# Performance work log

Measured on AMD Instinct MI355X. Metric: run time of the kernel, lower is better.

Reference implementation:

```python
import jax, jax.numpy as jnp
import numpy as np

T, N, K, E = 5, 2048, 20, 512
H, AI, BL, G1, G2, U = 64, 32, 64, 64, 64, 8
SLOPE, ALPHA = 0.01, 1.0


def gru(x, Wih, Whh, bih, bhh):
    # batch_first torch nn.GRU with h0 = 0. x: [B, L, I] -> [B, L, Hd]
    Hd = Whh.shape[1]
    def step(h, xt):
        gi = xt @ Wih.T + bih
        gh = h @ Whh.T + bhh
        ir, iz, in_ = jnp.split(gi, 3, axis=-1)
        hr, hz, hn = jnp.split(gh, 3, axis=-1)
        r = jax.nn.sigmoid(ir + hr)
        z = jax.nn.sigmoid(iz + hz)
        n = jnp.tanh(in_ + r * hn)
        h_new = (1.0 - z) * n + z * h
        return h_new, h_new
    h0 = jnp.zeros((x.shape[0], Hd), x.dtype)
    _, ys = jax.lax.scan(step, h0, jnp.swapaxes(x, 0, 1))
    return jnp.swapaxes(ys, 0, 1)


def lin_attn(x, w1, b1, w2):
    # LinearAttention: softmax over dim=2 (weights_size=1), then bmm -> [B,1,H]
    inter = jnp.tanh(x @ w1.T + b1)
    w = jax.nn.softmax(inter @ w2.T, axis=2)  # [B,L,1]
    return jnp.einsum('blk,blh->bkh', w, x)


def sgat_multi(x, W, a, adj):
    # All U SGAT heads at once. Decompose a^T [Wh_i || Wh_j] = s1_i + s2_j
    # (same math as the dense NxNx2F construction, without materializing it).
    O = W.shape[-1]
    Wh = jnp.einsum('nf,ufo->uno', x, W)                 # [U,N,O]
    s1 = jnp.einsum('uno,uo->un', Wh, a[:, :O, 0])
    s2 = jnp.einsum('uno,uo->un', Wh, a[:, O:, 0])
    e = jax.nn.leaky_relu(s1[:, :, None] + s2[:, None, :], SLOPE)  # [U,N,N]
    e = jnp.where(adj[None, :, :] > 0, e, -9e15)
    att = jax.nn.softmax(e, axis=2)
    h = jnp.einsum('unm,umo->uno', att, Wh)              # [U,N,O]
    # torch.cat over heads along feature dim -> [N, U*O]
    return jnp.transpose(h, (1, 0, 2)).reshape(x.shape[0], -1)


def setup_inputs() -> dict:
    key = jax.random.key(0)
    ks = iter(jax.random.split(key, 40))
    def nrm(shape, scale=0.1):
        return jax.random.normal(next(ks), shape, dtype=jnp.float32) * scale
    d = {}
    d['p'] = nrm((N, T, 3), 1.0)
    d['m'] = nrm((T, N, K, E), 1.0)
    adj = (jax.random.uniform(next(ks), (N, N)) < 0.05).astype(jnp.float32)
    d['adj'] = jnp.maximum(adj, jnp.eye(N, dtype=jnp.float32))
    d['Wih_p'] = nrm((3 * H, 3)); d['Whh_p'] = nrm((3 * H, H))
    d['bih_p'] = nrm((3 * H,)); d['bhh_p'] = nrm((3 * H,))
    d['Wih_m'] = nrm((3 * H, E)); d['Whh_m'] = nrm((3 * H, H))
    d['bih_m'] = nrm((3 * H,)); d['bhh_m'] = nrm((3 * H,))
    d['Wih_s'] = nrm((3 * H, H)); d['Whh_s'] = nrm((3 * H, H))
    d['bih_s'] = nrm((3 * H,)); d['bhh_s'] = nrm((3 * H,))
    for pref in ('ap', 'am', 'as'):
        d[pref + '_w1'] = nrm((AI, H)); d[pref + '_b1'] = nrm((AI,))
        d[pref + '_w2'] = nrm((1, AI))
    d['blend_W'] = nrm((BL, H, H)); d['blend_b'] = nrm((BL,))
    d['g1_W'] = nrm((U, BL, G1)); d['g1_a'] = nrm((U, 2 * G1, 1))
    d['g2_W'] = nrm((U, U * G1, G2)); d['g2_a'] = nrm((U, 2 * G2, 1))
    d['fin_W'] = nrm((1, U * G2)); d['fin_b'] = nrm((1,))
    return d


def reference(p, m, adj, Wih_p, Whh_p, bih_p, bhh_p, Wih_m, Whh_m, bih_m, bhh_m,
              Wih_s, Whh_s, bih_s, bhh_s, ap_w1, ap_b1, ap_w2, am_w1, am_b1, am_w2,
              as_w1, as_b1, as_w2, blend_W, blend_b, g1_W, g1_a, g2_W, g2_a,
              fin_W, fin_b):
    h_p = gru(p, Wih_p, Whh_p, bih_p, bhh_p)                     # [N,T,H]
    q = lin_attn(h_p, ap_w1, ap_b1, ap_w2)                       # [N,1,H]
    # all T message-days through gru_m at once (equivalent to python loop)
    h_m = gru(m.reshape(T * N, K, E), Wih_m, Whh_m, bih_m, bhh_m)
    r = lin_attn(h_m, am_w1, am_b1, am_w2).reshape(T, N, H).transpose(1, 0, 2)
    h_s = gru(r, Wih_s, Whh_s, bih_s, bhh_s)                     # [N,T,H]
    c = lin_attn(h_s, as_w1, as_b1, as_w2)                       # [N,1,H]
    # Blend: bilinear + relu
    x = jax.nn.relu(jnp.einsum('nbi,oij,nbj->nbo', q, blend_W, c) + blend_b)
    x = x.reshape(N, BL)
    z = jax.nn.elu(sgat_multi(x, g1_W, g1_a, adj), ALPHA)        # [N,U*G1]
    new_z = jax.nn.sigmoid(sgat_multi(z, g2_W, g2_a, adj))       # [N,U*G2]
    return jax.nn.sigmoid(new_z @ fin_W.T + fin_b)               # [N,1]
```

## Files before the change

### kernel.cpp

```cpp
#include <hip/hip_runtime.h>
#include <math.h>

namespace {

constexpr int T = 5, N = 2048, K = 20, E = 512;
constexpr int H = 64, U = 8;
constexpr int CAP = 512;
constexpr float SLOPE = 0.01f;

typedef __attribute__((ext_vector_type(8))) short short8;
typedef __attribute__((ext_vector_type(4))) float f32x4;

__device__ inline float sigm(float x) { return 1.0f / (1.0f + expf(-x)); }

__device__ inline void bsplit(float x, short& hi, short& lo) {
  unsigned u = __float_as_uint(x);
  hi = (short)(u >> 16);
  float r = x - __uint_as_float(u & 0xFFFF0000u);
  lo = (short)(__float_as_uint(r) >> 16);
}

__device__ inline float rdlane(float v, int lane) {
  return __int_as_float(__builtin_amdgcn_readlane(__float_as_int(v), lane));
}

__device__ inline void pack512(const float* __restrict__ src, short* __restrict__ dst,
                               const int Ksz, const int pb, const int nPB) {
  const int nb64 = Ksz >> 6;
  const int total = 8 * Ksz * 64;
  for (int idx = threadIdx.x + pb * 256; idx < total; idx += 256 * nPB) {
    const int u = idx / (Ksz * 64), rem = idx - u * Ksz * 64;
    const int f = rem >> 6, o = rem & 63;
    const int col = u * 64 + o;
    const long base = ((long)(col >> 7) * nb64 + (f >> 6)) * 8192
                    + (((f >> 5) & 1) * 8 + ((col >> 4) & 7)) * 512
                    + ((f >> 3) & 3) * 128 + (col & 15) * 8 + (f & 7);
    dst[base] = (short)(__float_as_uint(src[idx]) >> 16);
  }
}

__global__ __launch_bounds__(256) void k_prep_all(
    const float* __restrict__ WihM, const float* __restrict__ WhhM,
    const float* __restrict__ WihS, const float* __restrict__ WhhS,
    const float* __restrict__ WhhP, const float* __restrict__ Wb,
    const float* __restrict__ g1W, const float* __restrict__ g2W,
    const float* __restrict__ adj,
    short* __restrict__ BfM, short* __restrict__ BfS,
    short* __restrict__ Bf1, short* __restrict__ Bf2,
    float* __restrict__ WhhTm, float* __restrict__ WhhTs, float* __restrict__ WhhTp,
    float* __restrict__ Wt2, int* __restrict__ nbr, int* __restrict__ deg)
{
  const int b = blockIdx.x;
  if (b < N / 4) {
    const int w = threadIdx.x >> 6, lane = threadIdx.x & 63;
    const int i = b * 4 + w;
    int base = 0;
    for (int j0 = 0; j0 < N; j0 += 64) {
      const float v = adj[(long)i * N + j0 + lane];
      const unsigned long long mask = __ballot(v > 0.f);
      const int pre = __popcll(mask & ((1ull << lane) - 1ull));
      if (v > 0.f && base + pre < CAP) nbr[i * CAP + base + pre] = j0 + lane;
      base += __popcll(mask);
    }
    if (lane == 0) deg[i] = base < CAP ? base : CAP;
    return;
  }
  const int pb = b - N / 4;
  constexpr int NPB = 128;
  for (int idx = threadIdx.x + pb * 256; idx < 192 * 512; idx += 256 * NPB) {
    const int o = idx >> 9, k = idx & 511;
    const long base = (long)(k >> 6) * 12288 + (((k >> 5) & 1) * 12 + (o >> 4)) * 512
                    + ((k >> 3) & 3) * 128 + (o & 15) * 8 + (k & 7);
    BfM[base] = (short)(__float_as_uint(WihM[idx]) >> 16);
  }
  for (int idx = threadIdx.x + pb * 256; idx < 192 * 64; idx += 256 * NPB) {
    const int o = idx >> 6, k = idx & 63;
    const long base = (((k >> 5) & 1) * 12 + (o >> 4)) * 512
                    + ((k >> 3) & 3) * 128 + (o & 15) * 8 + (k & 7);
    BfS[base] = (short)(__float_as_uint(WihS[idx]) >> 16);
  }
  for (int idx = threadIdx.x + pb * 256; idx < 64 * 192; idx += 256 * NPB) {
    const int k2 = idx / 192, row = idx % 192;
    WhhTm[idx] = WhhM[row * 64 + k2];
    WhhTs[idx] = WhhS[row * 64 + k2];
    WhhTp[idx] = WhhP[row * 64 + k2];
  }
  for (int idx = threadIdx.x + pb * 256; idx < 64 * 64 * 64; idx += 256 * NPB) {
    const int o = idx >> 12, rem = idx & 4095, i = rem >> 6, j = rem & 63;
    Wt2[((i * 16 + (j >> 2)) * 64 + o) * 4 + (j & 3)] = Wb[(o * 64 + i) * 64 + j];
  }
  pack512(g1W, Bf1, 64, pb, NPB);
  pack512(g2W, Bf2, 512, pb, NPB);
}

__global__ __launch_bounds__(256, 3) void k_gemm(
    const float* __restrict__ A, const short* __restrict__ Bf,
    const float* __restrict__ bias, float* __restrict__ out,
    const long row0, const int nb, const int strideA)
{
  __shared__ alignas(16) short Bc[2][24 * 512];
  const int tid = threadIdx.x, w = tid >> 6, l = tid & 63;
  const int lr = l & 15, g = l >> 4;
  const long blkrow = (long)blockIdx.x * 128;

  f32x4 acc[2][12];
  #pragma unroll
  for (int mf = 0; mf < 2; ++mf)
    #pragma unroll
    for (int nt = 0; nt < 12; ++nt) acc[mf][nt] = (f32x4){0.f, 0.f, 0.f, 0.f};

  auto STAGE = [&](int buf, int b) {
    const short* __restrict__ bsrc = Bf + (long)b * 12288;
    #pragma unroll
    for (int i = 0; i < 6; ++i) {
      const int c = w + i * 4;
      __builtin_amdgcn_global_load_lds(
          (const __attribute__((address_space(1))) void*)(bsrc + c * 512 + l * 8),
          (__attribute__((address_space(3))) void*)(&Bc[buf][c * 512]), 16, 0, 0);
    }
  };

  STAGE(0, 0);
  __syncthreads();

  for (int b = 0; b < nb; ++b) {
    if (b + 1 < nb) STAGE((b + 1) & 1, b + 1);
    short8 ah[2][2], al[2][2];
    #pragma unroll
    for (int kc = 0; kc < 2; ++kc)
      #pragma unroll
      for (int mf = 0; mf < 2; ++mf) {
        const long r = blkrow + w * 32 + mf * 16 + lr;
        const float* __restrict__ src = A + (row0 + r) * (long)strideA + b * 64 + kc * 32 + g * 8;
        const float4 v0 = *reinterpret_cast<const float4*>(src);
        const float4 v1 = *reinterpret_cast<const float4*>(src + 4);
        short h0,l0,h1,l1,h2,l2,h3,l3,h4,l4,h5,l5,h6,l6,h7,l7;
        bsplit(v0.x,h0,l0); bsplit(v0.y,h1,l1); bsplit(v0.z,h2,l2); bsplit(v0.w,h3,l3);
        bsplit(v1.x,h4,l4); bsplit(v1.y,h5,l5); bsplit(v1.z,h6,l6); bsplit(v1.w,h7,l7);
        ah[kc][mf] = (short8){h0,h1,h2,h3,h4,h5,h6,h7};
        al[kc][mf] = (short8){l0,l1,l2,l3,l4,l5,l6,l7};
      }
    const short* __restrict__ bcur = &Bc[b & 1][0];
    #pragma unroll
    for (int kc = 0; kc < 2; ++kc) {
      #pragma unroll
      for (int nt = 0; nt < 12; ++nt) {
        const short8 bh = *reinterpret_cast<const short8*>(bcur + (kc * 12 + nt) * 512 + l * 8);
        #pragma unroll
        for (int mf = 0; mf < 2; ++mf) {
          acc[mf][nt] = __builtin_amdgcn_mfma_f32_16x16x32_bf16(ah[kc][mf], bh, acc[mf][nt], 0, 0, 0);
          acc[mf][nt] = __builtin_amdgcn_mfma_f32_16x16x32_bf16(al[kc][mf], bh, acc[mf][nt], 0, 0, 0);
        }
      }
    }
    __syncthreads();
  }

  #pragma unroll
  for (int mf = 0; mf < 2; ++mf) {
    const long rbase = blkrow + w * 32 + mf * 16 + g * 4;
    #pragma unroll
    for (int nt = 0; nt < 12; ++nt) {
      const int col = nt * 16 + lr;
      const float bb = bias[col];
      #pragma unroll
      for (int i = 0; i < 4; ++i)
        out[(rbase + i) * 192 + col] = acc[mf][nt][i] + bb;
    }
  }
}

__global__ __launch_bounds__(256, 3) void k_gemmW(
    const float* __restrict__ A, const short* __restrict__ Bf2,
    const float* __restrict__ ga,
    float* __restrict__ Wh, float* __restrict__ s1, float* __restrict__ s2,
    const int nb, const int strideA)
{
  __shared__ alignas(16) short Bc[2][16 * 512];
  const int tid = threadIdx.x, w = tid >> 6, l = tid & 63;
  const int lr = l & 15, g = l >> 4;
  const long blkrow = (long)blockIdx.x * 64;
  const int cb = blockIdx.y;

  f32x4 acc[8];
  #pragma unroll
  for (int nt = 0; nt < 8; ++nt) acc[nt] = (f32x4){0.f, 0.f, 0.f, 0.f};

  auto STAGE = [&](int buf, int b) {
    const short* __restrict__ bsrc = Bf2 + ((long)cb * nb + b) * 8192;
    #pragma unroll
    for (int i = 0; i < 4; ++i) {
      const int c = w + i * 4;
      __builtin_amdgcn_global_load_lds(
          (const __attribute__((address_space(1))) void*)(bsrc + c * 512 + l * 8),
          (__attribute__((address_space(3))) void*)(&Bc[buf][c * 512]), 16, 0, 0);
    }
  };

  STAGE(0, 0);
  __syncthreads();

  for (int b = 0; b < nb; ++b) {
    if (b + 1 < nb) STAGE((b + 1) & 1, b + 1);
    short8 ah[2], al[2];
    #pragma unroll
    for (int kc = 0; kc < 2; ++kc) {
      const long r = blkrow + w * 16 + lr;
      const float* __restrict__ src = A + r * (long)strideA + b * 64 + kc * 32 + g * 8;
      const float4 v0 = *reinterpret_cast<const float4*>(src);
      const float4 v1 = *reinterpret_cast<const float4*>(src + 4);
      short h0,l0,h1,l1,h2,l2,h3,l3,h4,l4,h5,l5,h6,l6,h7,l7;
      bsplit(v0.x,h0,l0); bsplit(v0.y,h1,l1); bsplit(v0.z,h2,l2); bsplit(v0.w,h3,l3);
      bsplit(v1.x,h4,l4); bsplit(v1.y,h5,l5); bsplit(v1.z,h6,l6); bsplit(v1.w,h7,l7);
      ah[kc] = (short8){h0,h1,h2,h3,h4,h5,h6,h7};
      al[kc] = (short8){l0,l1,l2,l3,l4,l5,l6,l7};
    }
    const short* __restrict__ bcur = &Bc[b & 1][0];
    #pragma unroll
    for (int kc = 0; kc < 2; ++kc) {
      #pragma unroll
      for (int nt = 0; nt < 8; ++nt) {
        const short8 bh = *reinterpret_cast<const short8*>(bcur + (kc * 8 + nt) * 512 + l * 8);
        acc[nt] = __builtin_amdgcn_mfma_f32_16x16x32_bf16(ah[kc], bh, acc[nt], 0, 0, 0);
        acc[nt] = __builtin_amdgcn_mfma_f32_16x16x32_bf16(al[kc], bh, acc[nt], 0, 0, 0);
      }
    }
    __syncthreads();
  }

  const long rbase = blkrow + w * 16 + g * 4;
  #pragma unroll
  for (int nt = 0; nt < 8; ++nt) {
    const int col = cb * 128 + nt * 16 + lr;
    const int u = col >> 6, o = col & 63;
    #pragma unroll
    for (int i = 0; i < 4; ++i)
      Wh[((long)u * N + (rbase + i)) * 64 + o] = acc[nt][i];
  }
  #pragma unroll
  for (int i = 0; i < 4; ++i) {
    const long r = rbase + i;
    #pragma unroll
    for (int uh = 0; uh < 2; ++uh) {
      const int u = cb * 2 + uh;
      float p1 = 0.f, p2 = 0.f;
      #pragma unroll
      for (int nt4 = 0; nt4 < 4; ++nt4) {
        const float v = acc[uh * 4 + nt4][i];
        const int o = nt4 * 16 + lr;
        p1 += v * ga[u * 128 + o];
        p2 += v * ga[u * 128 + 64 + o];
      }
      #pragma unroll
      for (int dd = 8; dd > 0; dd >>= 1) { p1 += __shfl_xor(p1, dd, 64); p2 += __shfl_xor(p2, dd, 64); }
      if (lr == 0) { s1[u * N + r] = p1; s2[u * N + r] = p2; }
    }
  }
}

__global__ __launch_bounds__(256, 2) void k_recur(
    const float* __restrict__ gi, const float* __restrict__ WhhT,
    const float* __restrict__ bhh, float* __restrict__ rout, const int seq0)
{
  const int tid = threadIdx.x, w = tid >> 6, l = tid & 63;
  const int lseq = blockIdx.x * 4 + w;
  float wr[64], wz[64], wn[64];
  #pragma unroll
  for (int k2 = 0; k2 < 64; ++k2) {
    wr[k2] = WhhT[k2 * 192 + l];
    wz[k2] = WhhT[k2 * 192 + 64 + l];
    wn[k2] = WhhT[k2 * 192 + 128 + l];
  }
  const float bR = bhh[l], bZ = bhh[64 + l], bN = bhh[128 + l];
  const float* __restrict__ grow = gi + (long)lseq * K * 192;
  float h = 0.f, rsum = 0.f;
  float gR = grow[l], gZ = grow[64 + l], gN = grow[128 + l];
  for (int k = 0; k < K; ++k) {
    float nR = 0.f, nZ = 0.f, nN = 0.f;
    if (k + 1 < K) {
      const int off = (k + 1) * 192;
      nR = grow[off + l]; nZ = grow[off + 64 + l]; nN = grow[off + 128 + l];
    }
    float aR = bR, aZ = bZ, aN = bN;
    #pragma unroll
    for (int k2 = 0; k2 < 64; ++k2) {
      const float hk = rdlane(h, k2);
      aR += wr[k2] * hk; aZ += wz[k2] * hk; aN += wn[k2] * hk;
    }
    const float r = sigm(gR + aR);
    const float z = sigm(gZ + aZ);
    const float nn = tanhf(gN + r * aN);
    h = (1.f - z) * nn + z * h;
    rsum += h;
    gR = nR; gZ = nZ; gN = nN;
  }
  const int gseq = seq0 + lseq;
  const int tt = gseq / N, n = gseq % N;
  rout[(n * T + tt) * H + l] = rsum;
}

__global__ __launch_bounds__(256, 2) void k_recur_p(
    const float* __restrict__ p, const float* __restrict__ Wih,
    const float* __restrict__ WhhT, const float* __restrict__ bih,
    const float* __restrict__ bhh, float* __restrict__ q)
{
  const int tid = threadIdx.x, w = tid >> 6, l = tid & 63;
  const int n = blockIdx.x * 4 + w;
  float wr[64], wz[64], wn[64];
  #pragma unroll
  for (int k2 = 0; k2 < 64; ++k2) {
    wr[k2] = WhhT[k2 * 192 + l];
    wz[k2] = WhhT[k2 * 192 + 64 + l];
    wn[k2] = WhhT[k2 * 192 + 128 + l];
  }
  float iR[3], iZ[3], iN[3];
  #pragma unroll
  for (int c = 0; c < 3; ++c) {
    iR[c] = Wih[l * 3 + c];
    iZ[c] = Wih[(64 + l) * 3 + c];
    iN[c] = Wih[(128 + l) * 3 + c];
  }
  const float biR = bih[l], biZ = bih[64 + l], biN = bih[128 + l];
  const float bhR = bhh[l], bhZ = bhh[64 + l], bhN = bhh[128 + l];
  float h = 0.f, qs = 0.f;
  for (int t = 0; t < T; ++t) {
    const float x0 = p[n * 15 + t * 3], x1 = p[n * 15 + t * 3 + 1], x2 = p[n * 15 + t * 3 + 2];
    const float gR = biR + iR[0] * x0 + iR[1] * x1 + iR[2] * x2;
    const float gZ = biZ + iZ[0] * x0 + iZ[1] * x1 + iZ[2] * x2;
    const float gN = biN + iN[0] * x0 + iN[1] * x1 + iN[2] * x2;
    float aR = bhR, aZ = bhZ, aN = bhN;
    #pragma unroll
    for (int k2 = 0; k2 < 64; ++k2) {
      const float hk = rdlane(h, k2);
      aR += wr[k2] * hk; aZ += wz[k2] * hk; aN += wn[k2] * hk;
    }
    const float r = sigm(gR + aR), z = sigm(gZ + aZ);
    const float nn = tanhf(gN + r * aN);
    h = (1.f - z) * nn + z * h;
    qs += h;
  }
  q[n * H + l] = qs;
}

__global__ __launch_bounds__(256, 2) void k_recur_s(
    const float* __restrict__ gx, const float* __restrict__ WhhT,
    const float* __restrict__ bhh, float* __restrict__ c)
{
  const int tid = threadIdx.x, w = tid >> 6, l = tid & 63;
  const int n = blockIdx.x * 4 + w;
  float wr[64], wz[64], wn[64];
  #pragma unroll
  for (int k2 = 0; k2 < 64; ++k2) {
    wr[k2] = WhhT[k2 * 192 + l];
    wz[k2] = WhhT[k2 * 192 + 64 + l];
    wn[k2] = WhhT[k2 * 192 + 128 + l];
  }
  const float bR = bhh[l], bZ = bhh[64 + l], bN = bhh[128 + l];
  const float* __restrict__ grow = gx + (long)n * T * 192;
  float h = 0.f, cs = 0.f;
  for (int t = 0; t < T; ++t) {
    const float gR = grow[t * 192 + l], gZ = grow[t * 192 + 64 + l], gN = grow[t * 192 + 128 + l];
    float aR = bR, aZ = bZ, aN = bN;
    #pragma unroll
    for (int k2 = 0; k2 < 64; ++k2) {
      const float hk = rdlane(h, k2);
      aR += wr[k2] * hk; aZ += wz[k2] * hk; aN += wn[k2] * hk;
    }
    const float r = sigm(gR + aR), z = sigm(gZ + aZ);
    const float nn = tanhf(gN + r * aN);
    h = (1.f - z) * nn + z * h;
    cs += h;
  }
  c[n * H + l] = cs;
}

__global__ __launch_bounds__(256) void k_blend(
    const float* __restrict__ q, const float* __restrict__ c,
    const float* __restrict__ Wt2, const float* __restrict__ b,
    float* __restrict__ xout)
{
  __shared__ float qs[8][64];
  __shared__ alignas(16) float cs[8][64];
  const int tid = threadIdx.x;
  const int o = tid & 63, grp = tid >> 6;
  const int n0 = blockIdx.x * 8;
  for (int idx = tid; idx < 512; idx += 256) {
    qs[idx >> 6][idx & 63] = q[(n0 + (idx >> 6)) * 64 + (idx & 63)];
    cs[idx >> 6][idx & 63] = c[(n0 + (idx >> 6)) * 64 + (idx & 63)];
  }
  __syncthreads();
  const int na = grp * 2, nb = na + 1;
  float acca = b[o], accb = b[o];
  const float4* __restrict__ W4 = reinterpret_cast<const float4*>(Wt2);
  const float4* ca4 = reinterpret_cast<const float4*>(&cs[na][0]);
  const float4* cb4 = reinterpret_cast<const float4*>(&cs[nb][0]);
  for (int i = 0; i < 64; ++i) {
    float pa = 0.f, pb = 0.f;
    #pragma unroll
    for (int j4 = 0; j4 < 16; ++j4) {
      const float4 wv = W4[(i * 16 + j4) * 64 + o];
      const float4 va = ca4[j4], vb = cb4[j4];
      pa += wv.x * va.x + wv.y * va.y + wv.z * va.z + wv.w * va.w;
      pb += wv.x * vb.x + wv.y * vb.y + wv.z * vb.z + wv.w * vb.w;
    }
    acca += qs[na][i] * pa;
    accb += qs[nb][i] * pb;
  }
  xout[(n0 + na) * 64 + o] = fmaxf(acca, 0.f);
  xout[(n0 + nb) * 64 + o] = fmaxf(accb, 0.f);
}

__global__ __launch_bounds__(256) void k_gat_attn(
    const float* __restrict__ Wh, const float* __restrict__ s1,
    const float* __restrict__ s2, const int* __restrict__ nbr,
    const int* __restrict__ deg, const int mode, float* __restrict__ out)
{
  __shared__ float ew[4][CAP];
  __shared__ int nb[4][CAP];
  const int w = threadIdx.x >> 6, lane = threadIdx.x & 63;
  const int row = blockIdx.x * 4 + w;
  const int u = row >> 11;
  const int i = row & (N - 1);
  const int d = deg[i];
  const float su = s1[u * N + i];
  float mx = -1e30f;
  for (int t = lane; t < d; t += 64) {
    const int j = nbr[i * CAP + t];
    float e = su + s2[u * N + j];
    e = e > 0.f ? e : SLOPE * e;
    ew[w][t] = e; nb[w][t] = j;
    mx = fmaxf(mx, e);
  }
  #pragma unroll
  for (int dd = 32; dd > 0; dd >>= 1) mx = fmaxf(mx, __shfl_xor(mx, dd, 64));
  float sm = 0.f;
  for (int t = lane; t < d; t += 64) {
    const float ex = expf(ew[w][t] - mx);
    ew[w][t] = ex;
    sm += ex;
  }
  #pragma unroll
  for (int dd = 32; dd > 0; dd >>= 1) sm += __shfl_xor(sm, dd, 64);
  __syncthreads();
  const float inv = 1.f / sm;
  float a0 = 0.f, a1 = 0.f, a2 = 0.f, a3 = 0.f;
  const float* __restrict__ whb = Wh + (long)u * N * 64 + lane;
  int t = 0;
  for (; t + 4 <= d; t += 4) {
    const float e0 = ew[w][t],     e1 = ew[w][t + 1];
    const float e2 = ew[w][t + 2], e3 = ew[w][t + 3];
    const int j0 = nb[w][t],     j1 = nb[w][t + 1];
    const int j2 = nb[w][t + 2], j3 = nb[w][t + 3];
    a0 += e0 * whb[(long)j0 * 64];
    a1 += e1 * whb[(long)j1 * 64];
    a2 += e2 * whb[(long)j2 * 64];
    a3 += e3 * whb[(long)j3 * 64];
  }
  for (; t < d; ++t) a0 += ew[w][t] * whb[(long)nb[w][t] * 64];
  float acc = ((a0 + a1) + (a2 + a3)) * inv;
  float val;
  if (mode == 0) val = acc > 0.f ? acc : (expf(acc) - 1.f);
  else           val = 1.f / (1.f + expf(-acc));
  out[(long)i * (U * 64) + u * 64 + lane] = val;
}

__global__ __launch_bounds__(256) void k_final(
    const float* __restrict__ nz, const float* __restrict__ fw,
    const float* __restrict__ fb, float* __restrict__ out)
{
  const int w = threadIdx.x >> 6, lane = threadIdx.x & 63;
  const int n = blockIdx.x * 4 + w;
  float p = 0.f;
  #pragma unroll
  for (int f = lane; f < 512; f += 64) p += nz[(long)n * 512 + f] * fw[f];
  #pragma unroll
  for (int d = 32; d > 0; d >>= 1) p += __shfl_xor(p, d, 64);
  if (lane == 0) out[n] = 1.f / (1.f + expf(-(p + fb[0])));
}

}

extern "C" void kernel_launch(void* const* d_in, const int* in_sizes, int n_in,
                              void* d_out, int out_size, void* d_ws, size_t ws_size,
                              hipStream_t stream)
{
  const float* p     = (const float*)d_in[0];
  const float* m     = (const float*)d_in[1];
  const float* adj   = (const float*)d_in[2];
  const float* Wih_p = (const float*)d_in[3];
  const float* Whh_p = (const float*)d_in[4];
  const float* bih_p = (const float*)d_in[5];
  const float* bhh_p = (const float*)d_in[6];
  const float* Wih_m = (const float*)d_in[7];
  const float* Whh_m = (const float*)d_in[8];
  const float* bih_m = (const float*)d_in[9];
  const float* bhh_m = (const float*)d_in[10];
  const float* Wih_s = (const float*)d_in[11];
  const float* Whh_s = (const float*)d_in[12];
  const float* bih_s = (const float*)d_in[13];
  const float* bhh_s = (const float*)d_in[14];
  const float* blend_W = (const float*)d_in[24];
  const float* blend_b = (const float*)d_in[25];
  const float* g1W = (const float*)d_in[26];
  const float* g1a = (const float*)d_in[27];
  const float* g2W = (const float*)d_in[28];
  const float* g2a = (const float*)d_in[29];
  const float* finW = (const float*)d_in[30];
  const float* finb = (const float*)d_in[31];

  float* ws = (float*)d_ws;
  float* q    = ws;
  float* rr   = q + N * H;
  float* c    = rr + N * T * H;
  float* xb   = c + N * H;
  float* Wh1  = xb + N * H;
  float* s1a  = Wh1 + U * N * 64;
  float* s2a  = s1a + U * N;
  float* z    = s2a + U * N;
  float* Wh2  = z + (long)N * 512;
  float* s1b  = Wh2 + U * N * 64;
  float* s2b  = s1b + U * N;
  float* nz   = s2b + U * N;
  float* Wt2  = nz + (long)N * 512;
  float* gx   = Wt2 + 64 * 64 * 64;
  float* WhhTm = gx + (long)10240 * 192;
  float* WhhTs = WhhTm + 64 * 192;
  float* WhhTp = WhhTs + 64 * 192;
  int*   nbr  = (int*)(WhhTp + 64 * 192);
  int*   deg  = nbr + (long)N * CAP;
  short* BfM  = (short*)(deg + N);
  short* BfS  = BfM + 8 * 12288;
  short* Bf1  = BfS + 12288;
  short* Bf2  = Bf1 + 4 * 8192;
  float* gi   = (float*)(Bf2 + 4 * 8 * 8192);

  const long avail = (long)(ws_size / 4) - (gi - ws);
  const long total_seqs = (long)T * N;
  long chunk = (avail / ((long)K * 192) / 32) * 32;
  if (chunk > total_seqs) chunk = total_seqs;
  if (chunk < 32) chunk = 32;

  k_prep_all<<<N / 4 + 128, 256, 0, stream>>>(
      Wih_m, Whh_m, Wih_s, Whh_s, Whh_p, blend_W, g1W, g2W, adj,
      BfM, BfS, Bf1, Bf2, WhhTm, WhhTs, WhhTp, Wt2, nbr, deg);
  k_recur_p<<<N / 4, 256, 0, stream>>>(p, Wih_p, WhhTp, bih_p, bhh_p, q);
  for (long s0 = 0; s0 < total_seqs; s0 += chunk) {
    const long cs = (total_seqs - s0) < chunk ? (total_seqs - s0) : chunk;
    const long rows = cs * K;
    k_gemm<<<(int)(rows / 128), 256, 0, stream>>>(m, BfM, bih_m, gi, s0 * K, 8, 512);
    k_recur<<<(int)(cs / 4), 256, 0, stream>>>(gi, WhhTm, bhh_m, rr, (int)s0);
  }
  k_gemm<<<80, 256, 0, stream>>>(rr, BfS, bih_s, gx, 0, 1, 64);
  k_recur_s<<<N / 4, 256, 0, stream>>>(gx, WhhTs, bhh_s, c);
  k_blend<<<N / 8, 256, 0, stream>>>(q, c, Wt2, blend_b, xb);
  k_gemmW<<<dim3(N / 64, 4), 256, 0, stream>>>(xb, Bf1, g1a, Wh1, s1a, s2a, 1, 64);
  k_gat_attn<<<(U * N) / 4, 256, 0, stream>>>(Wh1, s1a, s2a, nbr, deg, 0, z);
  k_gemmW<<<dim3(N / 64, 4), 256, 0, stream>>>(z, Bf2, g2a, Wh2, s1b, s2b, 8, 512);
  k_gat_attn<<<(U * N) / 4, 256, 0, stream>>>(Wh2, s1b, s2b, nbr, deg, 1, nz);
  k_final<<<N / 4, 256, 0, stream>>>(nz, finW, finb, (float*)d_out);
}
```

Measured before the change: 465.3 us.

## Fold p-GRU recurrence into prep kernel and prefetch A tiles in GEMMs

Removes the separate k_recur_p launch and runs the p-stream GRU as extra blocks of k_prep_all, reading Whh_p directly in row-major order instead of a transposed copy. The A-operand loads in k_gemm and k_gemmW are now software-prefetched into registers one k-block ahead, so global load latency can overlap the MFMA work. k_gemm launch bounds drop from 3 to 2 waves per EU to make room for the extra prefetch registers. The trade-off is lower occupancy, and the prep kernel becomes heavier and mixes register-hungry recurrence blocks with packing blocks.

```diff
diff --git a/kernel.cpp b/kernel.cpp
--- a/kernel.cpp
+++ b/kernel.cpp
@@ -45,10 +45,13 @@
     const float* __restrict__ WhhP, const float* __restrict__ Wb,
     const float* __restrict__ g1W, const float* __restrict__ g2W,
     const float* __restrict__ adj,
+    const float* __restrict__ p, const float* __restrict__ WihP,
+    const float* __restrict__ bihP, const float* __restrict__ bhhP,
     short* __restrict__ BfM, short* __restrict__ BfS,
     short* __restrict__ Bf1, short* __restrict__ Bf2,
-    float* __restrict__ WhhTm, float* __restrict__ WhhTs, float* __restrict__ WhhTp,
-    float* __restrict__ Wt2, int* __restrict__ nbr, int* __restrict__ deg)
+    float* __restrict__ WhhTm, float* __restrict__ WhhTs,
+    float* __restrict__ Wt2, int* __restrict__ nbr, int* __restrict__ deg,
+    float* __restrict__ q)
 {
   const int b = blockIdx.x;
   if (b < N / 4) {
@@ -65,35 +68,74 @@
     if (lane == 0) deg[i] = base < CAP ? base : CAP;
     return;
   }
-  const int pb = b - N / 4;
-  constexpr int NPB = 128;
-  for (int idx = threadIdx.x + pb * 256; idx < 192 * 512; idx += 256 * NPB) {
-    const int o = idx >> 9, k = idx & 511;
-    const long base = (long)(k >> 6) * 12288 + (((k >> 5) & 1) * 12 + (o >> 4)) * 512
-                    + ((k >> 3) & 3) * 128 + (o & 15) * 8 + (k & 7);
-    BfM[base] = (short)(__float_as_uint(WihM[idx]) >> 16);
-  }
-  for (int idx = threadIdx.x + pb * 256; idx < 192 * 64; idx += 256 * NPB) {
-    const int o = idx >> 6, k = idx & 63;
-    const long base = (((k >> 5) & 1) * 12 + (o >> 4)) * 512
-                    + ((k >> 3) & 3) * 128 + (o & 15) * 8 + (k & 7);
-    BfS[base] = (short)(__float_as_uint(WihS[idx]) >> 16);
-  }
-  for (int idx = threadIdx.x + pb * 256; idx < 64 * 192; idx += 256 * NPB) {
-    const int k2 = idx / 192, row = idx % 192;
-    WhhTm[idx] = WhhM[row * 64 + k2];
-    WhhTs[idx] = WhhS[row * 64 + k2];
-    WhhTp[idx] = WhhP[row * 64 + k2];
-  }
-  for (int idx = threadIdx.x + pb * 256; idx < 64 * 64 * 64; idx += 256 * NPB) {
-    const int o = idx >> 12, rem = idx & 4095, i = rem >> 6, j = rem & 63;
-    Wt2[((i * 16 + (j >> 2)) * 64 + o) * 4 + (j & 3)] = Wb[(o * 64 + i) * 64 + j];
-  }
-  pack512(g1W, Bf1, 64, pb, NPB);
-  pack512(g2W, Bf2, 512, pb, NPB);
-}
-
-__global__ __launch_bounds__(256, 3) void k_gemm(
+  if (b < N / 4 + 128) {
+    const int pb = b - N / 4;
+    constexpr int NPB = 128;
+    for (int idx = threadIdx.x + pb * 256; idx < 192 * 512; idx += 256 * NPB) {
+      const int o = idx >> 9, k = idx & 511;
+      const long base = (long)(k >> 6) * 12288 + (((k >> 5) & 1) * 12 + (o >> 4)) * 512
+                      + ((k >> 3) & 3) * 128 + (o & 15) * 8 + (k & 7);
+      BfM[base] = (short)(__float_as_uint(WihM[idx]) >> 16);
+    }
+    for (int idx = threadIdx.x + pb * 256; idx < 192 * 64; idx += 256 * NPB) {
+      const int o = idx >> 6, k = idx & 63;
+      const long base = (((k >> 5) & 1) * 12 + (o >> 4)) * 512
+                      + ((k >> 3) & 3) * 128 + (o & 15) * 8 + (k & 7);
+      BfS[base] = (short)(__float_as_uint(WihS[idx]) >> 16);
+    }
+    for (int idx = threadIdx.x + pb * 256; idx < 64 * 192; idx += 256 * NPB) {
+      const int k2 = idx / 192, row = idx % 192;
+      WhhTm[idx] = WhhM[row * 64 + k2];
+      WhhTs[idx] = WhhS[row * 64 + k2];
+    }
+    for (int idx = threadIdx.x + pb * 256; idx < 64 * 64 * 64; idx += 256 * NPB) {
+      const int o = idx >> 12, rem = idx & 4095, i = rem >> 6, j = rem & 63;
+      Wt2[((i * 16 + (j >> 2)) * 64 + o) * 4 + (j & 3)] = Wb[(o * 64 + i) * 64 + j];
+    }
+    pack512(g1W, Bf1, 64, pb, NPB);
+    pack512(g2W, Bf2, 512, pb, NPB);
+    return;
+  }
+  const int rb = b - (N / 4 + 128);
+  const int w = threadIdx.x >> 6, l = threadIdx.x & 63;
+  const int n = rb * 4 + w;
+  float wr[64], wz[64], wn[64];
+  #pragma unroll
+  for (int k2 = 0; k2 < 64; ++k2) {
+    wr[k2] = WhhP[l * 64 + k2];
+    wz[k2] = WhhP[(64 + l) * 64 + k2];
+    wn[k2] = WhhP[(128 + l) * 64 + k2];
+  }
+  float iR[3], iZ[3], iN[3];
+  #pragma unroll
+  for (int c = 0; c < 3; ++c) {
+    iR[c] = WihP[l * 3 + c];
+    iZ[c] = WihP[(64 + l) * 3 + c];
+    iN[c] = WihP[(128 + l) * 3 + c];
+  }
+  const float biR = bihP[l], biZ = bihP[64 + l], biN = bihP[128 + l];
+  const float bhR = bhhP[l], bhZ = bhhP[64 + l], bhN = bhhP[128 + l];
+  float h = 0.f, qs = 0.f;
+  for (int t = 0; t < T; ++t) {
+    const float x0 = p[n * 15 + t * 3], x1 = p[n * 15 + t * 3 + 1], x2 = p[n * 15 + t * 3 + 2];
+    const float gR = biR + iR[0] * x0 + iR[1] * x1 + iR[2] * x2;
+    const float gZ = biZ + iZ[0] * x0 + iZ[1] * x1 + iZ[2] * x2;
+    const float gN = biN + iN[0] * x0 + iN[1] * x1 + iN[2] * x2;
+    float aR = bhR, aZ = bhZ, aN = bhN;
+    #pragma unroll
+    for (int k2 = 0; k2 < 64; ++k2) {
+      const float hk = rdlane(h, k2);
+      aR += wr[k2] * hk; aZ += wz[k2] * hk; aN += wn[k2] * hk;
+    }
+    const float r = sigm(gR + aR), z = sigm(gZ + aZ);
+    const float nn = tanhf(gN + r * aN);
+    h = (1.f - z) * nn + z * h;
+    qs += h;
+  }
+  q[n * H + l] = qs;
+}
+
+__global__ __launch_bounds__(256, 2) void k_gemm(
     const float* __restrict__ A, const short* __restrict__ Bf,
     const float* __restrict__ bias, float* __restrict__ out,
     const long row0, const int nb, const int strideA)
@@ -109,6 +151,19 @@
     #pragma unroll
     for (int nt = 0; nt < 12; ++nt) acc[mf][nt] = (f32x4){0.f, 0.f, 0.f, 0.f};
 
+  float4 pf[2][2][2];
+
+  auto LOADA = [&](int b) {
+    #pragma unroll
+    for (int kc = 0; kc < 2; ++kc)
+      #pragma unroll
+      for (int mf = 0; mf < 2; ++mf) {
+        const long r = blkrow + w * 32 + mf * 16 + lr;
+        const float* __restrict__ src = A + (row0 + r) * (long)strideA + b * 64 + kc * 32 + g * 8;
+        pf[kc][mf][0] = *reinterpret_cast<const float4*>(src);
+        pf[kc][mf][1] = *reinterpret_cast<const float4*>(src + 4);
+      }
+  };
   auto STAGE = [&](int buf, int b) {
     const short* __restrict__ bsrc = Bf + (long)b * 12288;
     #pragma unroll
@@ -121,25 +176,25 @@
   };
 
   STAGE(0, 0);
+  LOADA(0);
   __syncthreads();
 
   for (int b = 0; b < nb; ++b) {
-    if (b + 1 < nb) STAGE((b + 1) & 1, b + 1);
+    const bool more = (b + 1 < nb);
+    if (more) STAGE((b + 1) & 1, b + 1);
     short8 ah[2][2], al[2][2];
     #pragma unroll
     for (int kc = 0; kc < 2; ++kc)
       #pragma unroll
       for (int mf = 0; mf < 2; ++mf) {
-        const long r = blkrow + w * 32 + mf * 16 + lr;
-        const float* __restrict__ src = A + (row0 + r) * (long)strideA + b * 64 + kc * 32 + g * 8;
-        const float4 v0 = *reinterpret_cast<const float4*>(src);
-        const float4 v1 = *reinterpret_cast<const float4*>(src + 4);
+        const float4 v0 = pf[kc][mf][0], v1 = pf[kc][mf][1];
         short h0,l0,h1,l1,h2,l2,h3,l3,h4,l4,h5,l5,h6,l6,h7,l7;
         bsplit(v0.x,h0,l0); bsplit(v0.y,h1,l1); bsplit(v0.z,h2,l2); bsplit(v0.w,h3,l3);
         bsplit(v1.x,h4,l4); bsplit(v1.y,h5,l5); bsplit(v1.z,h6,l6); bsplit(v1.w,h7,l7);
         ah[kc][mf] = (short8){h0,h1,h2,h3,h4,h5,h6,h7};
         al[kc][mf] = (short8){l0,l1,l2,l3,l4,l5,l6,l7};
       }
+    if (more) LOADA(b + 1);
     const short* __restrict__ bcur = &Bc[b & 1][0];
     #pragma unroll
     for (int kc = 0; kc < 2; ++kc) {
@@ -186,6 +241,17 @@
   #pragma unroll
   for (int nt = 0; nt < 8; ++nt) acc[nt] = (f32x4){0.f, 0.f, 0.f, 0.f};
 
+  float4 pf[2][2];
+
+  auto LOADA = [&](int b) {
+    #pragma unroll
+    for (int kc = 0; kc < 2; ++kc) {
+      const long r = blkrow + w * 16 + lr;
+      const float* __restrict__ src = A + r * (long)strideA + b * 64 + kc * 32 + g * 8;
+      pf[kc][0] = *reinterpret_cast<const float4*>(src);
+      pf[kc][1] = *reinterpret_cast<const float4*>(src + 4);
+    }
+  };
   auto STAGE = [&](int buf, int b) {
     const short* __restrict__ bsrc = Bf2 + ((long)cb * nb + b) * 8192;
     #pragma unroll
@@ -198,23 +264,23 @@
   };
 
   STAGE(0, 0);
+  LOADA(0);
   __syncthreads();
 
   for (int b = 0; b < nb; ++b) {
-    if (b + 1 < nb) STAGE((b + 1) & 1, b + 1);
+    const bool more = (b + 1 < nb);
+    if (more) STAGE((b + 1) & 1, b + 1);
     short8 ah[2], al[2];
     #pragma unroll
     for (int kc = 0; kc < 2; ++kc) {
-      const long r = blkrow + w * 16 + lr;
-      const float* __restrict__ src = A + r * (long)strideA + b * 64 + kc * 32 + g * 8;
-      const float4 v0 = *reinterpret_cast<const float4*>(src);
-      const float4 v1 = *reinterpret_cast<const float4*>(src + 4);
+      const float4 v0 = pf[kc][0], v1 = pf[kc][1];
       short h0,l0,h1,l1,h2,l2,h3,l3,h4,l4,h5,l5,h6,l6,h7,l7;
       bsplit(v0.x,h0,l0); bsplit(v0.y,h1,l1); bsplit(v0.z,h2,l2); bsplit(v0.w,h3,l3);
       bsplit(v1.x,h4,l4); bsplit(v1.y,h5,l5); bsplit(v1.z,h6,l6); bsplit(v1.w,h7,l7);
       ah[kc] = (short8){h0,h1,h2,h3,h4,h5,h6,h7};
       al[kc] = (short8){l0,l1,l2,l3,l4,l5,l6,l7};
     }
+    if (more) LOADA(b + 1);
     const short* __restrict__ bcur = &Bc[b & 1][0];
     #pragma unroll
     for (int kc = 0; kc < 2; ++kc) {
@@ -297,49 +363,6 @@
   const int gseq = seq0 + lseq;
   const int tt = gseq / N, n = gseq % N;
   rout[(n * T + tt) * H + l] = rsum;
-}
-
-__global__ __launch_bounds__(256, 2) void k_recur_p(
-    const float* __restrict__ p, const float* __restrict__ Wih,
-    const float* __restrict__ WhhT, const float* __restrict__ bih,
-    const float* __restrict__ bhh, float* __restrict__ q)
-{
-  const int tid = threadIdx.x, w = tid >> 6, l = tid & 63;
-  const int n = blockIdx.x * 4 + w;
-  float wr[64], wz[64], wn[64];
-  #pragma unroll
-  for (int k2 = 0; k2 < 64; ++k2) {
-    wr[k2] = WhhT[k2 * 192 + l];
-    wz[k2] = WhhT[k2 * 192 + 64 + l];
-    wn[k2] = WhhT[k2 * 192 + 128 + l];
-  }
-  float iR[3], iZ[3], iN[3];
-  #pragma unroll
-  for (int c = 0; c < 3; ++c) {
-    iR[c] = Wih[l * 3 + c];
-    iZ[c] = Wih[(64 + l) * 3 + c];
-    iN[c] = Wih[(128 + l) * 3 + c];
-  }
-  const float biR = bih[l], biZ = bih[64 + l], biN = bih[128 + l];
-  const float bhR = bhh[l], bhZ = bhh[64 + l], bhN = bhh[128 + l];
-  float h = 0.f, qs = 0.f;
-  for (int t = 0; t < T; ++t) {
-    const float x0 = p[n * 15 + t * 3], x1 = p[n * 15 + t * 3 + 1], x2 = p[n * 15 + t * 3 + 2];
-    const float gR = biR + iR[0] * x0 + iR[1] * x1 + iR[2] * x2;
-    const float gZ = biZ + iZ[0] * x0 + iZ[1] * x1 + iZ[2] * x2;
-    const float gN = biN + iN[0] * x0 + iN[1] * x1 + iN[2] * x2;
-    float aR = bhR, aZ = bhZ, aN = bhN;
-    #pragma unroll
-    for (int k2 = 0; k2 < 64; ++k2) {
-      const float hk = rdlane(h, k2);
-      aR += wr[k2] * hk; aZ += wz[k2] * hk; aN += wn[k2] * hk;
-    }
-    const float r = sigm(gR + aR), z = sigm(gZ + aZ);
-    const float nn = tanhf(gN + r * aN);
-    h = (1.f - z) * nn + z * h;
-    qs += h;
-  }
-  q[n * H + l] = qs;
 }
 
 __global__ __launch_bounds__(256, 2) void k_recur_s(
@@ -525,8 +548,7 @@
   float* gx   = Wt2 + 64 * 64 * 64;
   float* WhhTm = gx + (long)10240 * 192;
   float* WhhTs = WhhTm + 64 * 192;
-  float* WhhTp = WhhTs + 64 * 192;
-  int*   nbr  = (int*)(WhhTp + 64 * 192);
+  int*   nbr  = (int*)(WhhTs + 64 * 192);
   int*   deg  = nbr + (long)N * CAP;
   short* BfM  = (short*)(deg + N);
   short* BfS  = BfM + 8 * 12288;
@@ -540,10 +562,10 @@
   if (chunk > total_seqs) chunk = total_seqs;
   if (chunk < 32) chunk = 32;
 
-  k_prep_all<<<N / 4 + 128, 256, 0, stream>>>(
+  k_prep_all<<<N / 4 + 128 + N / 4, 256, 0, stream>>>(
       Wih_m, Whh_m, Wih_s, Whh_s, Whh_p, blend_W, g1W, g2W, adj,
-      BfM, BfS, Bf1, Bf2, WhhTm, WhhTs, WhhTp, Wt2, nbr, deg);
-  k_recur_p<<<N / 4, 256, 0, stream>>>(p, Wih_p, WhhTp, bih_p, bhh_p, q);
+      p, Wih_p, bih_p, bhh_p,
+      BfM, BfS, Bf1, Bf2, WhhTm, WhhTs, Wt2, nbr, deg, q);
   for (long s0 = 0; s0 < total_seqs; s0 += chunk) {
     const long cs = (total_seqs - s0) < chunk ? (total_seqs - s0) : chunk;
     const long rows = cs * K;
```

After: 449.8 us (median of 3 runs). -3.3%, faster.
